# Optimization experiments

Measured on AMD Instinct MI355X. Metric: run time of the kernel, lower is better.

## Reference

```python
import jax, jax.numpy as jnp
import numpy as np

RESOLUTIONS = [16, 29, 53, 98, 181, 332, 610, 1120]
FEATURE_DIM = 4
FEATURE_STD = 0.01
BATCH = 4
NUM_SAMPLES = 524288


def setup_inputs() -> dict:
    key = jax.random.key(0)
    keys = jax.random.split(key, len(RESOLUTIONS) + 1)
    coords = jax.random.uniform(keys[0], (BATCH, NUM_SAMPLES, 2), dtype=jnp.float32,
                                minval=-1.0, maxval=1.0)
    inp = {"coords": coords, "lod_idx": len(RESOLUTIONS) - 1}
    for i, (res, k) in enumerate(zip(RESOLUTIONS, keys[1:])):
        inp[f"cb{i}"] = jax.random.normal(k, (FEATURE_DIM, res, res), jnp.float32) * FEATURE_STD
    return inp


def _bilerp(cb, coords, align_corners=True):
    """Bilinear grid_sample of cb [F,R,R] at coords [B,N,2] in [-1,1]. Returns [B,N,F]."""
    res = cb.shape[-1]
    if align_corners:
        p = (coords + 1.0) * 0.5 * (res - 1)  # pixel-space coords
    else:
        p = (coords + 1.0) * 0.5 * res - 0.5
    px, py = p[..., 0], p[..., 1]  # x = width idx, y = height idx (grid_sample convention)
    x0f = jnp.floor(px)
    y0f = jnp.floor(py)
    wx = px - x0f  # [B,N]
    wy = py - y0f
    x0 = jnp.clip(x0f.astype(jnp.int32), 0, res - 1)
    x1 = jnp.clip(x0f.astype(jnp.int32) + 1, 0, res - 1)
    y0 = jnp.clip(y0f.astype(jnp.int32), 0, res - 1)
    y1 = jnp.clip(y0f.astype(jnp.int32) + 1, 0, res - 1)
    # Gathers: advanced indexing on last two axes -> [F, B, N]
    f00 = cb[:, y0, x0]
    f01 = cb[:, y0, x1]
    f10 = cb[:, y1, x0]
    f11 = cb[:, y1, x1]
    w00 = ((1.0 - wx) * (1.0 - wy))[None]
    w01 = (wx * (1.0 - wy))[None]
    w10 = ((1.0 - wx) * wy)[None]
    w11 = (wx * wy)[None]
    out = f00 * w00 + f01 * w01 + f10 * w10 + f11 * w11  # [F,B,N]
    return jnp.moveaxis(out, 0, -1)  # [B,N,F]


def reference(coords, lod_idx, cb0, cb1, cb2, cb3, cb4, cb5, cb6, cb7):
    # lod_idx == max lod: all LODs active. multiscale_type='cat'.
    cbs = [cb0, cb1, cb2, cb3, cb4, cb5, cb6, cb7][: lod_idx + 1]
    feats = [_bilerp(cb, coords, align_corners=True) for cb in cbs]
    return jnp.concatenate(feats, axis=-1)  # [B, N, num_lods*feature_dim]
```

## Files before the change

### kernel.cpp

```cpp
#include <hip/hip_runtime.h>
#include <hip/hip_fp16.h>

#define NLEVELS 8
#define NBANDS  64
#define CHUNK   1024

__constant__ int   c_res[NLEVELS]   = {16, 29, 53, 98, 181, 332, 610, 1120};
__constant__ float c_scale[NLEVELS] = {7.5f, 14.0f, 26.0f, 48.5f, 90.0f, 165.5f, 304.5f, 559.5f};
__constant__ int   c_cum[NLEVELS]   = {0, 256, 1097, 3906, 13510, 46271, 156495, 528595};
#define TOTAL_TEXELS 1782995

typedef float        f32x4 __attribute__((ext_vector_type(4)));
typedef float        f32x2 __attribute__((ext_vector_type(2)));
typedef unsigned int u32;
typedef u32          u32x4 __attribute__((ext_vector_type(4), aligned(8)));

struct CbPtrs { const float* cb[NLEVELS]; };

__device__ __forceinline__ float2 up_h2(u32 v) {
    __half2 h = *reinterpret_cast<__half2*>(&v);
    return __half22float2(h);
}

__device__ __forceinline__ int band_of(float cy) {
    float v = (cy + 1.0f) * 0.5f;
    int k = (int)(v * (float)NBANDS);
    return min(NBANDS - 1, max(0, k));
}

__global__ __launch_bounds__(256) void transpose_cbs(CbPtrs p, uint2* __restrict__ tcb, int total) {
    for (int t = blockIdx.x * blockDim.x + threadIdx.x; t < total; t += gridDim.x * blockDim.x) {
        int L = 0;
#pragma unroll
        for (int i = 1; i < NLEVELS; ++i) if (t >= c_cum[i]) L = i;
        int i  = t - c_cum[L];
        int rr = c_res[L] * c_res[L];
        const float* cb = p.cb[L];
        __half2 h01 = __floats2half2_rn(cb[i],          cb[i + rr]);
        __half2 h23 = __floats2half2_rn(cb[i + 2 * rr], cb[i + 3 * rr]);
        uint2 tex;
        tex.x = *reinterpret_cast<u32*>(&h01);
        tex.y = *reinterpret_cast<u32*>(&h23);
        tcb[t] = tex;
    }
}

__global__ __launch_bounds__(64) void zero_counts(u32* gcount) {
    gcount[threadIdx.x] = 0u;
}

__global__ __launch_bounds__(256) void hist_kernel(const float2* __restrict__ coords,
                                                   u32* __restrict__ gcount, int S) {
    __shared__ u32 h[NBANDS];
    for (int i = threadIdx.x; i < NBANDS; i += 256) h[i] = 0u;
    __syncthreads();
    for (int s = blockIdx.x * 256 + threadIdx.x; s < S; s += gridDim.x * 256)
        atomicAdd(&h[band_of(coords[s].y)], 1u);
    __syncthreads();
    for (int i = threadIdx.x; i < NBANDS; i += 256)
        if (h[i]) atomicAdd(&gcount[i], h[i]);
}

__global__ __launch_bounds__(64) void scan_kernel(const u32* __restrict__ gcount,
                                                  u32* __restrict__ gcursor) {
    if (threadIdx.x == 0) {
        u32 acc = 0;
        for (int i = 0; i < NBANDS; ++i) { gcursor[i] = acc; acc += gcount[i]; }
    }
}

__global__ __launch_bounds__(256) void scatter_kernel(const float2* __restrict__ coords,
                                                      u32* __restrict__ gcursor,
                                                      float2* __restrict__ coordsS,
                                                      int*    __restrict__ idxS, int S) {
    __shared__ u32 h[NBANDS];
    __shared__ u32 rank_base[NBANDS];
    int s0 = blockIdx.x * CHUNK;
    for (int i = threadIdx.x; i < NBANDS; i += 256) h[i] = 0u;
    __syncthreads();
    u32 myrank[CHUNK / 256];
    int myk[CHUNK / 256];
    float2 myc[CHUNK / 256];
#pragma unroll
    for (int it = 0; it < CHUNK / 256; ++it) {
        int s = s0 + it * 256 + threadIdx.x;
        if (s < S) {
            float2 c = coords[s];
            int k = band_of(c.y);
            myc[it] = c;
            myk[it] = k;
            myrank[it] = atomicAdd(&h[k], 1u);
        }
    }
    __syncthreads();
    for (int i = threadIdx.x; i < NBANDS; i += 256)
        rank_base[i] = h[i] ? atomicAdd(&gcursor[i], h[i]) : 0u;
    __syncthreads();
#pragma unroll
    for (int it = 0; it < CHUNK / 256; ++it) {
        int s = s0 + it * 256 + threadIdx.x;
        if (s < S) {
            u32 pos = rank_base[myk[it]] + myrank[it];
            coordsS[pos] = myc[it];
            idxS[pos]    = s;
        }
    }
}

__global__ __launch_bounds__(256) void grid_sorted8(const f32x2* __restrict__ coordsS,
                                                    const int*   __restrict__ idxS,
                                                    const uint2* __restrict__ tcb,
                                                    f32x4* __restrict__ out, int S) {
    int p  = blockIdx.x;
    int nb = gridDim.x;
    int b  = (p & 7) * (nb >> 3) + (p >> 3);
    int t  = b * 256 + threadIdx.x;
    int s  = t >> 3;
    if (s >= S) return;
    int L  = t & 7;

    f32x2 c = coordsS[s];
    int idx = idxS[s];

    int   res   = c_res[L];
    float scale = c_scale[L];
    const uint2* __restrict__ base = tcb + c_cum[L];

    float px = (c.x + 1.0f) * scale;
    float py = (c.y + 1.0f) * scale;
    float xf = floorf(px), yf = floorf(py);
    float wx = px - xf,    wy = py - yf;
    int x0 = (int)xf, y0 = (int)yf;
    int xp = min(max(x0, 0), res - 2);  wx += (float)(x0 - xp);
    int yp = min(max(y0, 0), res - 2);  wy += (float)(y0 - yp);
    const uint2* r0 = base + yp * res + xp;
    u32x4 t0 = *(const u32x4*)r0;
    u32x4 t1 = *(const u32x4*)(r0 + res);

    float2 a00 = up_h2(t0.x), b00 = up_h2(t0.y);
    float2 a01 = up_h2(t0.z), b01 = up_h2(t0.w);
    float2 a10 = up_h2(t1.x), b10 = up_h2(t1.y);
    float2 a11 = up_h2(t1.z), b11 = up_h2(t1.w);

    float w00 = (1.0f - wx) * (1.0f - wy);
    float w01 = wx * (1.0f - wy);
    float w10 = (1.0f - wx) * wy;
    float w11 = wx * wy;

    f32x4 r;
    r.x = a00.x * w00 + a01.x * w01 + a10.x * w10 + a11.x * w11;
    r.y = a00.y * w00 + a01.y * w01 + a10.y * w10 + a11.y * w11;
    r.z = b00.x * w00 + b01.x * w01 + b10.x * w10 + b11.x * w11;
    r.w = b00.y * w00 + b01.y * w01 + b10.y * w10 + b11.y * w11;

    out[(size_t)idx * 8 + L] = r;
}

__global__ __launch_bounds__(256) void grid_main(const float2* __restrict__ coords,
                                                 const uint2* __restrict__ tcb,
                                                 f32x4* __restrict__ out4, int S) {
    int t = blockIdx.x * 256 + threadIdx.x;
    if (t >= S * 8) return;
    int L = t & 7;
    int s = t >> 3;
    float2 c = coords[s];
    int   res   = c_res[L];
    float scale = c_scale[L];
    const uint2* __restrict__ base = tcb + c_cum[L];
    float px = (c.x + 1.0f) * scale;
    float py = (c.y + 1.0f) * scale;
    float xf = floorf(px), yf = floorf(py);
    float wx = px - xf,    wy = py - yf;
    int x0 = (int)xf, y0 = (int)yf;
    int xp = min(max(x0, 0), res - 2);  wx += (float)(x0 - xp);
    int yp = min(max(y0, 0), res - 2);  wy += (float)(y0 - yp);
    const uint2* r0 = base + yp * res + xp;
    u32x4 t0 = *(const u32x4*)r0;
    u32x4 t1 = *(const u32x4*)(r0 + res);
    float2 a00 = up_h2(t0.x), b00 = up_h2(t0.y);
    float2 a01 = up_h2(t0.z), b01 = up_h2(t0.w);
    float2 a10 = up_h2(t1.x), b10 = up_h2(t1.y);
    float2 a11 = up_h2(t1.z), b11 = up_h2(t1.w);
    float w00 = (1.0f - wx) * (1.0f - wy);
    float w01 = wx * (1.0f - wy);
    float w10 = (1.0f - wx) * wy;
    float w11 = wx * wy;
    f32x4 r;
    r.x = a00.x * w00 + a01.x * w01 + a10.x * w10 + a11.x * w11;
    r.y = a00.y * w00 + a01.y * w01 + a10.y * w10 + a11.y * w11;
    r.z = b00.x * w00 + b01.x * w01 + b10.x * w10 + b11.x * w11;
    r.w = b00.y * w00 + b01.y * w01 + b10.y * w10 + b11.y * w11;
    out4[t] = r;
}

__global__ __launch_bounds__(256) void grid_generic(const float2* __restrict__ coords,
                                                    CbPtrs p, float4* __restrict__ out4,
                                                    int S, int levels) {
    int s = blockIdx.x * 256 + threadIdx.x;
    if (s >= S) return;
    float2 c = coords[s];
    for (int L = 0; L < levels; ++L) {
        int   res   = c_res[L];
        float scale = c_scale[L];
        float px = (c.x + 1.0f) * scale;
        float py = (c.y + 1.0f) * scale;
        float x0f = floorf(px), y0f = floorf(py);
        float wx = px - x0f,    wy = py - y0f;
        int rm1 = res - 1;
        int x0 = min(max((int)x0f, 0), rm1);
        int x1 = min(x0 + 1, rm1);
        int y0 = min(max((int)y0f, 0), rm1);
        int y1 = min(y0 + 1, rm1);
        int i00 = y0 * res + x0, i01 = y0 * res + x1, i10 = y1 * res + x0, i11 = y1 * res + x1;
        float w00 = (1.0f - wx) * (1.0f - wy);
        float w01 = wx * (1.0f - wy);
        float w10 = (1.0f - wx) * wy;
        float w11 = wx * wy;
        float4 r;
        const float* cb = p.cb[L];
        int rr = res * res;
        float* pr = &r.x;
#pragma unroll
        for (int f = 0; f < 4; ++f) {
            const float* cf = cb + f * rr;
            pr[f] = cf[i00] * w00 + cf[i01] * w01 + cf[i10] * w10 + cf[i11] * w11;
        }
        out4[(size_t)s * levels + L] = r;
    }
}

extern "C" void kernel_launch(void* const* d_in, const int* in_sizes, int n_in,
                              void* d_out, int out_size, void* d_ws, size_t ws_size,
                              hipStream_t stream) {
    const float2* coords = (const float2*)d_in[0];
    int S = in_sizes[0] / 2;
    int levels = out_size / (S * 4);

    CbPtrs ptrs;
    for (int i = 0; i < NLEVELS; ++i) ptrs.cb[i] = (const float*)d_in[2 + i];

    size_t tcb_bytes  = ((size_t)TOTAL_TEXELS * 8 + 255) & ~(size_t)255;
    size_t cnt_bytes  = 1024;
    size_t crd_bytes  = (size_t)S * 8;
    size_t idx_bytes  = (size_t)S * 4;
    size_t need_sorted = tcb_bytes + cnt_bytes + crd_bytes + idx_bytes;

    char* ws = (char*)d_ws;
    uint2*  tcb     = (uint2*)ws;
    u32*    gcount  = (u32*)(ws + tcb_bytes);
    u32*    gcursor = gcount + NBANDS;
    float2* coordsS = (float2*)(ws + tcb_bytes + cnt_bytes);
    int*    idxS    = (int*)(ws + tcb_bytes + cnt_bytes + crd_bytes);

    if (levels != NLEVELS) {
        int blocks = (S + 255) / 256;
        grid_generic<<<blocks, 256, 0, stream>>>(coords, ptrs, (float4*)d_out, S, levels);
        return;
    }
    if (ws_size < tcb_bytes) {
        int blocks = (S + 255) / 256;
        grid_generic<<<blocks, 256, 0, stream>>>(coords, ptrs, (float4*)d_out, S, levels);
        return;
    }

    int tg = (TOTAL_TEXELS + 255) / 256;
    transpose_cbs<<<tg, 256, 0, stream>>>(ptrs, tcb, TOTAL_TEXELS);

    if (ws_size >= need_sorted) {
        int nchunk = (S + CHUNK - 1) / CHUNK;
        zero_counts<<<1, 64, 0, stream>>>(gcount);
        hist_kernel<<<512, 256, 0, stream>>>(coords, gcount, S);
        scan_kernel<<<1, 64, 0, stream>>>(gcount, gcursor);
        scatter_kernel<<<nchunk, 256, 0, stream>>>(coords, gcursor, coordsS, idxS, S);
        long long total = (long long)S * 8;
        int nb = (int)((total + 255) / 256);
        nb = ((nb + 7) / 8) * 8;
        grid_sorted8<<<nb, 256, 0, stream>>>((const f32x2*)coordsS, idxS, tcb, (f32x4*)d_out, S);
    } else {
        long long total = (long long)S * 8;
        int blocks = (int)((total + 255) / 256);
        grid_main<<<blocks, 256, 0, stream>>>(coords, tcb, (f32x4*)d_out, S);
    }
}
```

Measured before the change: 179.3 us.

## Pre-expand quad table for small levels and fuse histogram into prep kernel

```diff
diff --git a/kernel.cpp b/kernel.cpp
--- a/kernel.cpp
+++ b/kernel.cpp
@@ -8,18 +8,27 @@
 __constant__ int   c_res[NLEVELS]   = {16, 29, 53, 98, 181, 332, 610, 1120};
 __constant__ float c_scale[NLEVELS] = {7.5f, 14.0f, 26.0f, 48.5f, 90.0f, 165.5f, 304.5f, 559.5f};
 __constant__ int   c_cum[NLEVELS]   = {0, 256, 1097, 3906, 13510, 46271, 156495, 528595};
-#define TOTAL_TEXELS 1782995
+#define QTOT    528595
+#define L7RES   1120
+#define L7TEX   (L7RES * L7RES)
+#define QTAB_BYTES   ((size_t)QTOT * 32)
+#define L7TAB_BYTES  ((size_t)L7TEX * 8)
 
 typedef float        f32x4 __attribute__((ext_vector_type(4)));
 typedef float        f32x2 __attribute__((ext_vector_type(2)));
 typedef unsigned int u32;
-typedef u32          u32x4 __attribute__((ext_vector_type(4), aligned(8)));
+typedef u32          u32x4a8 __attribute__((ext_vector_type(4), aligned(8)));
 
 struct CbPtrs { const float* cb[NLEVELS]; };
 
 __device__ __forceinline__ float2 up_h2(u32 v) {
     __half2 h = *reinterpret_cast<__half2*>(&v);
     return __half22float2(h);
+}
+
+__device__ __forceinline__ u32 pack_h2(float a, float b) {
+    __half2 h = __floats2half2_rn(a, b);
+    return *reinterpret_cast<u32*>(&h);
 }
 
 __device__ __forceinline__ int band_of(float cy) {
@@ -28,37 +37,62 @@
     return min(NBANDS - 1, max(0, k));
 }
 
-__global__ __launch_bounds__(256) void transpose_cbs(CbPtrs p, uint2* __restrict__ tcb, int total) {
-    for (int t = blockIdx.x * blockDim.x + threadIdx.x; t < total; t += gridDim.x * blockDim.x) {
-        int L = 0;
-#pragma unroll
-        for (int i = 1; i < NLEVELS; ++i) if (t >= c_cum[i]) L = i;
-        int i  = t - c_cum[L];
-        int rr = c_res[L] * c_res[L];
-        const float* cb = p.cb[L];
-        __half2 h01 = __floats2half2_rn(cb[i],          cb[i + rr]);
-        __half2 h23 = __floats2half2_rn(cb[i + 2 * rr], cb[i + 3 * rr]);
-        uint2 tex;
-        tex.x = *reinterpret_cast<u32*>(&h01);
-        tex.y = *reinterpret_cast<u32*>(&h23);
-        tcb[t] = tex;
+#define PREP_TBLOCKS 1024
+__global__ __launch_bounds__(256) void prep_kernel(CbPtrs p,
+                                                   uint2* __restrict__ qtab,
+                                                   uint2* __restrict__ l7tab,
+                                                   const float2* __restrict__ coords,
+                                                   u32* __restrict__ gcount, int S) {
+    if (blockIdx.x < PREP_TBLOCKS) {
+        const int total = QTOT + L7TEX;
+        for (int t = blockIdx.x * 256 + threadIdx.x; t < total; t += PREP_TBLOCKS * 256) {
+            if (t < QTOT) {
+                int L = 0;
+#pragma unroll
+                for (int i = 1; i < 7; ++i) if (t >= c_cum[i]) L = i;
+                int i   = t - c_cum[L];
+                int res = c_res[L];
+                int rr  = res * res;
+                int y   = i / res, x = i - y * res;
+                int xn  = min(x + 1, res - 1), yn = min(y + 1, res - 1);
+                const float* cb = p.cb[L];
+                int i00 = y * res + x,  i01 = y * res + xn;
+                int i10 = yn * res + x, i11 = yn * res + xn;
+                uint2 q0, q1, q2, q3;
+                q0.x = pack_h2(cb[i00], cb[i00 + rr]);
+                q0.y = pack_h2(cb[i00 + 2 * rr], cb[i00 + 3 * rr]);
+                q1.x = pack_h2(cb[i01], cb[i01 + rr]);
+                q1.y = pack_h2(cb[i01 + 2 * rr], cb[i01 + 3 * rr]);
+                q2.x = pack_h2(cb[i10], cb[i10 + rr]);
+                q2.y = pack_h2(cb[i10 + 2 * rr], cb[i10 + 3 * rr]);
+                q3.x = pack_h2(cb[i11], cb[i11 + rr]);
+                q3.y = pack_h2(cb[i11 + 2 * rr], cb[i11 + 3 * rr]);
+                uint2* q = qtab + 4 * (size_t)t;
+                q[0] = q0; q[1] = q1; q[2] = q2; q[3] = q3;
+            } else {
+                int i  = t - QTOT;
+                const float* cb = p.cb[7];
+                uint2 tex;
+                tex.x = pack_h2(cb[i], cb[i + L7TEX]);
+                tex.y = pack_h2(cb[i + 2 * L7TEX], cb[i + 3 * L7TEX]);
+                l7tab[i] = tex;
+            }
+        }
+    } else {
+        __shared__ u32 h[NBANDS];
+        for (int i = threadIdx.x; i < NBANDS; i += 256) h[i] = 0u;
+        __syncthreads();
+        int nb = gridDim.x - PREP_TBLOCKS;
+        for (int s = (blockIdx.x - PREP_TBLOCKS) * 256 + threadIdx.x; s < S; s += nb * 256)
+            atomicAdd(&h[band_of(coords[s].y)], 1u);
+        __syncthreads();
+        for (int i = threadIdx.x; i < NBANDS; i += 256)
+            if (h[i]) atomicAdd(&gcount[i], h[i]);
     }
 }
 
 __global__ __launch_bounds__(64) void zero_counts(u32* gcount) {
     gcount[threadIdx.x] = 0u;
-}
-
-__global__ __launch_bounds__(256) void hist_kernel(const float2* __restrict__ coords,
-                                                   u32* __restrict__ gcount, int S) {
-    __shared__ u32 h[NBANDS];
-    for (int i = threadIdx.x; i < NBANDS; i += 256) h[i] = 0u;
-    __syncthreads();
-    for (int s = blockIdx.x * 256 + threadIdx.x; s < S; s += gridDim.x * 256)
-        atomicAdd(&h[band_of(coords[s].y)], 1u);
-    __syncthreads();
-    for (int i = threadIdx.x; i < NBANDS; i += 256)
-        if (h[i]) atomicAdd(&gcount[i], h[i]);
 }
 
 __global__ __launch_bounds__(64) void scan_kernel(const u32* __restrict__ gcount,
@@ -109,7 +143,8 @@
 
 __global__ __launch_bounds__(256) void grid_sorted8(const f32x2* __restrict__ coordsS,
                                                     const int*   __restrict__ idxS,
-                                                    const uint2* __restrict__ tcb,
+                                                    const uint2* __restrict__ qtab,
+                                                    const uint2* __restrict__ l7tab,
                                                     f32x4* __restrict__ out, int S) {
     int p  = blockIdx.x;
     int nb = gridDim.x;
@@ -124,8 +159,6 @@
 
     int   res   = c_res[L];
     float scale = c_scale[L];
-    const uint2* __restrict__ base = tcb + c_cum[L];
-
     float px = (c.x + 1.0f) * scale;
     float py = (c.y + 1.0f) * scale;
     float xf = floorf(px), yf = floorf(py);
@@ -133,14 +166,22 @@
     int x0 = (int)xf, y0 = (int)yf;
     int xp = min(max(x0, 0), res - 2);  wx += (float)(x0 - xp);
     int yp = min(max(y0, 0), res - 2);  wy += (float)(y0 - yp);
-    const uint2* r0 = base + yp * res + xp;
-    u32x4 t0 = *(const u32x4*)r0;
-    u32x4 t1 = *(const u32x4*)(r0 + res);
-
-    float2 a00 = up_h2(t0.x), b00 = up_h2(t0.y);
-    float2 a01 = up_h2(t0.z), b01 = up_h2(t0.w);
-    float2 a10 = up_h2(t1.x), b10 = up_h2(t1.y);
-    float2 a11 = up_h2(t1.z), b11 = up_h2(t1.w);
+
+    u32x4a8 h0, h1;
+    if (L < 7) {
+        const u32x4a8* q = (const u32x4a8*)(qtab + 4 * (size_t)(c_cum[L] + yp * res + xp));
+        h0 = q[0];
+        h1 = q[1];
+    } else {
+        const uint2* r0 = l7tab + yp * L7RES + xp;
+        h0 = *(const u32x4a8*)r0;
+        h1 = *(const u32x4a8*)(r0 + L7RES);
+    }
+
+    float2 a00 = up_h2(h0.x), b00 = up_h2(h0.y);
+    float2 a01 = up_h2(h0.z), b01 = up_h2(h0.w);
+    float2 a10 = up_h2(h1.x), b10 = up_h2(h1.y);
+    float2 a11 = up_h2(h1.z), b11 = up_h2(h1.w);
 
     float w00 = (1.0f - wx) * (1.0f - wy);
     float w01 = wx * (1.0f - wy);
@@ -154,43 +195,6 @@
     r.w = b00.y * w00 + b01.y * w01 + b10.y * w10 + b11.y * w11;
 
     out[(size_t)idx * 8 + L] = r;
-}
-
-__global__ __launch_bounds__(256) void grid_main(const float2* __restrict__ coords,
-                                                 const uint2* __restrict__ tcb,
-                                                 f32x4* __restrict__ out4, int S) {
-    int t = blockIdx.x * 256 + threadIdx.x;
-    if (t >= S * 8) return;
-    int L = t & 7;
-    int s = t >> 3;
-    float2 c = coords[s];
-    int   res   = c_res[L];
-    float scale = c_scale[L];
-    const uint2* __restrict__ base = tcb + c_cum[L];
-    float px = (c.x + 1.0f) * scale;
-    float py = (c.y + 1.0f) * scale;
-    float xf = floorf(px), yf = floorf(py);
-    float wx = px - xf,    wy = py - yf;
-    int x0 = (int)xf, y0 = (int)yf;
-    int xp = min(max(x0, 0), res - 2);  wx += (float)(x0 - xp);
-    int yp = min(max(y0, 0), res - 2);  wy += (float)(y0 - yp);
-    const uint2* r0 = base + yp * res + xp;
-    u32x4 t0 = *(const u32x4*)r0;
-    u32x4 t1 = *(const u32x4*)(r0 + res);
-    float2 a00 = up_h2(t0.x), b00 = up_h2(t0.y);
-    float2 a01 = up_h2(t0.z), b01 = up_h2(t0.w);
-    float2 a10 = up_h2(t1.x), b10 = up_h2(t1.y);
-    float2 a11 = up_h2(t1.z), b11 = up_h2(t1.w);
-    float w00 = (1.0f - wx) * (1.0f - wy);
-    float w01 = wx * (1.0f - wy);
-    float w10 = (1.0f - wx) * wy;
-    float w11 = wx * wy;
-    f32x4 r;
-    r.x = a00.x * w00 + a01.x * w01 + a10.x * w10 + a11.x * w11;
-    r.y = a00.y * w00 + a01.y * w01 + a10.y * w10 + a11.y * w11;
-    r.z = b00.x * w00 + b01.x * w01 + b10.x * w10 + b11.x * w11;
-    r.w = b00.y * w00 + b01.y * w01 + b10.y * w10 + b11.y * w11;
-    out4[t] = r;
 }
 
 __global__ __launch_bounds__(256) void grid_generic(const float2* __restrict__ coords,
@@ -239,46 +243,34 @@
     CbPtrs ptrs;
     for (int i = 0; i < NLEVELS; ++i) ptrs.cb[i] = (const float*)d_in[2 + i];
 
-    size_t tcb_bytes  = ((size_t)TOTAL_TEXELS * 8 + 255) & ~(size_t)255;
+    size_t tab_bytes  = (QTAB_BYTES + L7TAB_BYTES + 255) & ~(size_t)255;
     size_t cnt_bytes  = 1024;
     size_t crd_bytes  = (size_t)S * 8;
     size_t idx_bytes  = (size_t)S * 4;
-    size_t need_sorted = tcb_bytes + cnt_bytes + crd_bytes + idx_bytes;
+    size_t need = tab_bytes + cnt_bytes + crd_bytes + idx_bytes;
 
     char* ws = (char*)d_ws;
-    uint2*  tcb     = (uint2*)ws;
-    u32*    gcount  = (u32*)(ws + tcb_bytes);
+    uint2*  qtab    = (uint2*)ws;
+    uint2*  l7tab   = (uint2*)(ws + QTAB_BYTES);
+    u32*    gcount  = (u32*)(ws + tab_bytes);
     u32*    gcursor = gcount + NBANDS;
-    float2* coordsS = (float2*)(ws + tcb_bytes + cnt_bytes);
-    int*    idxS    = (int*)(ws + tcb_bytes + cnt_bytes + crd_bytes);
-
-    if (levels != NLEVELS) {
+    float2* coordsS = (float2*)(ws + tab_bytes + cnt_bytes);
+    int*    idxS    = (int*)(ws + tab_bytes + cnt_bytes + crd_bytes);
+
+    if (levels != NLEVELS || ws_size < need) {
         int blocks = (S + 255) / 256;
         grid_generic<<<blocks, 256, 0, stream>>>(coords, ptrs, (float4*)d_out, S, levels);
         return;
     }
-    if (ws_size < tcb_bytes) {
-        int blocks = (S + 255) / 256;
-        grid_generic<<<blocks, 256, 0, stream>>>(coords, ptrs, (float4*)d_out, S, levels);
-        return;
-    }
-
-    int tg = (TOTAL_TEXELS + 255) / 256;
-    transpose_cbs<<<tg, 256, 0, stream>>>(ptrs, tcb, TOTAL_TEXELS);
-
-    if (ws_size >= need_sorted) {
-        int nchunk = (S + CHUNK - 1) / CHUNK;
-        zero_counts<<<1, 64, 0, stream>>>(gcount);
-        hist_kernel<<<512, 256, 0, stream>>>(coords, gcount, S);
-        scan_kernel<<<1, 64, 0, stream>>>(gcount, gcursor);
-        scatter_kernel<<<nchunk, 256, 0, stream>>>(coords, gcursor, coordsS, idxS, S);
-        long long total = (long long)S * 8;
-        int nb = (int)((total + 255) / 256);
-        nb = ((nb + 7) / 8) * 8;
-        grid_sorted8<<<nb, 256, 0, stream>>>((const f32x2*)coordsS, idxS, tcb, (f32x4*)d_out, S);
-    } else {
-        long long total = (long long)S * 8;
-        int blocks = (int)((total + 255) / 256);
-        grid_main<<<blocks, 256, 0, stream>>>(coords, tcb, (f32x4*)d_out, S);
-    }
-}
+
+    zero_counts<<<1, 64, 0, stream>>>(gcount);
+    prep_kernel<<<PREP_TBLOCKS + 512, 256, 0, stream>>>(ptrs, qtab, l7tab, coords, gcount, S);
+    scan_kernel<<<1, 64, 0, stream>>>(gcount, gcursor);
+    int nchunk = (S + CHUNK - 1) / CHUNK;
+    scatter_kernel<<<nchunk, 256, 0, stream>>>(coords, gcursor, coordsS, idxS, S);
+    long long total = (long long)S * 8;
+    int nb = (int)((total + 255) / 256);
+    nb = ((nb + 7) / 8) * 8;
+    grid_sorted8<<<nb, 256, 0, stream>>>((const f32x2*)coordsS, idxS, qtab, l7tab,
+                                         (f32x4*)d_out, S);
+}
```

New measurement: 181.0 us. Within noise of the previous version (+1.0%).
